# Optimization experiments

Hardware: AMD Instinct MI355X
Metric: run time of the kernel (lower is better)

Reference implementation:

```python
import jax, jax.numpy as jnp
import numpy as np

NUM_HEAD = 16
EMBED_DIM = 1024
HEAD_DIM = EMBED_DIM // NUM_HEAD
QK_DIM = EMBED_DIM  # qk_dim defaults to embed_dim


def setup_inputs() -> dict:
    key = jax.random.key(0)
    k1, k2, k3 = jax.random.split(key, 3)
    x = jax.random.normal(k1, (4, 2048, EMBED_DIM), dtype=jnp.float32)
    # xavier_uniform-like init scale
    lim_qkv = float(np.sqrt(6.0 / (EMBED_DIM + 3 * EMBED_DIM)))
    lim_out = float(np.sqrt(6.0 / (EMBED_DIM + EMBED_DIM)))
    W_QKV = jax.random.uniform(k2, (EMBED_DIM, 3 * EMBED_DIM), jnp.float32, -lim_qkv, lim_qkv)
    W_Out = jax.random.uniform(k3, (EMBED_DIM, EMBED_DIM), jnp.float32, -lim_out, lim_out)
    return {"x": x, "W_QKV": W_QKV, "W_Out": W_Out}


def reference(x, W_QKV, W_Out):
    bsz, slen, _ = x.shape
    # [b,s,3E] -> [b,s,H,hd,3] -> [b,H,s,hd,3]  (interleaved qkv layout, as in torch source)
    qkv = (x @ W_QKV).reshape(bsz, slen, NUM_HEAD, HEAD_DIM, 3).transpose(0, 2, 1, 3, 4)
    q, k, v = qkv[..., 0], qkv[..., 1], qkv[..., 2]
    # NOTE: module scales by sqrt(qk_dim) (full dim), not sqrt(head_dim)
    scores = jnp.einsum("bhqd,bhkd->bhqk", q, k) / np.sqrt(QK_DIM).astype(np.float32)
    attn = jax.nn.softmax(scores, axis=-1)  # dropout p=0.0 -> identity
    out = jnp.einsum("bhqk,bhkd->bhqd", attn, v)  # [b,H,s,hd]
    out = out.transpose(0, 2, 1, 3).reshape(bsz, slen, EMBED_DIM)
    return out @ W_Out
```

## Files before the change

kernel.cpp:

```cpp
#include <hip/hip_runtime.h>
#include <stdint.h>

typedef __bf16 bf16x8 __attribute__((ext_vector_type(8)));
typedef __bf16 bf16x4_t __attribute__((ext_vector_type(4)));
typedef float f32x4 __attribute__((ext_vector_type(4)));
typedef unsigned short u16x8 __attribute__((ext_vector_type(8)));
typedef unsigned short u16x4 __attribute__((ext_vector_type(4)));
typedef short s16x4 __attribute__((ext_vector_type(4)));
typedef unsigned int u32x2 __attribute__((ext_vector_type(2)));

#if __has_builtin(__builtin_amdgcn_mfma_f32_16x16x16bf16_1k)
#define MFMA16X16X16(a, b, c) __builtin_amdgcn_mfma_f32_16x16x16bf16_1k((a), (b), (c), 0, 0, 0)
#elif __has_builtin(__builtin_amdgcn_mfma_f32_16x16x16_bf16)
#define MFMA16X16X16(a, b, c)                                                             \
    __builtin_amdgcn_mfma_f32_16x16x16_bf16(__builtin_bit_cast(bf16x4_t, (a)),            \
                                            __builtin_bit_cast(bf16x4_t, (b)), (c), 0, 0, 0)
#else
static __device__ __forceinline__ f32x4 MFMA16X16X16(s16x4, s16x4, f32x4 c) { return c; }
#endif

#if __has_builtin(__builtin_amdgcn_exp2f)
#define EXP2(x) __builtin_amdgcn_exp2f(x)
#else
#define EXP2(x) exp2f(x)
#endif

__device__ __forceinline__ unsigned short f2bf(float f) {
    unsigned int u = __float_as_uint(f);
    u += 0x7fffu + ((u >> 16) & 1u);
    return (unsigned short)(u >> 16);
}

__device__ __forceinline__ int swz64(int row, int c) {
    return (c & 7) | ((((c >> 3) ^ row) & 7) << 3);
}

__device__ __forceinline__ void glds16(const unsigned short* g, unsigned short* l) {
    __builtin_amdgcn_global_load_lds((const __attribute__((address_space(1))) void*)g,
                                     (__attribute__((address_space(3))) void*)l, 16, 0, 0);
}

__device__ __forceinline__ void transpose_body(const float* __restrict__ in,
                                               unsigned short* __restrict__ out,
                                               unsigned short (*tile)[33],
                                               int K, int N, int permute, int nb, int kb) {
    int tx = threadIdx.x & 31, ty = threadIdx.x >> 5;
    #pragma unroll
    for (int r = ty; r < 32; r += 8)
        tile[r][tx] = f2bf(in[(size_t)(kb + r) * N + nb + tx]);
    __syncthreads();
    #pragma unroll
    for (int r = ty; r < 32; r += 8) {
        int n_orig = nb + r, col = kb + tx;
        int row;
        if (permute) {
            int h = n_orig / 192, rem = n_orig - h * 192;
            int d = rem / 3, cc = rem - 3 * d;
            row = cc * 1024 + h * 64 + d;
        } else {
            row = n_orig;
        }
        out[(size_t)row * K + (col & ~63) + swz64(row, col & 63)] = tile[tx][r];
    }
}

__global__ __launch_bounds__(256) void preprocess_kernel(const float* __restrict__ x,
                                                         const float* __restrict__ wqkv,
                                                         const float* __restrict__ wout,
                                                         unsigned short* __restrict__ xb,
                                                         unsigned short* __restrict__ wqkvt,
                                                         unsigned short* __restrict__ woutt) {
    __shared__ unsigned short tile[32][33];
    int bid = blockIdx.x;
    if (bid < 4096) {
        size_t id = (size_t)bid * 256 + threadIdx.x;
        int row = (int)(id >> 7);
        int cid = (int)(id & 127);
        const float4* src = (const float4*)(x + id * 8);
        float4 a = src[0], b = src[1];
        u16x8 o;
        o[0] = f2bf(a.x); o[1] = f2bf(a.y); o[2] = f2bf(a.z); o[3] = f2bf(a.w);
        o[4] = f2bf(b.x); o[5] = f2bf(b.y); o[6] = f2bf(b.z); o[7] = f2bf(b.w);
        int group = cid >> 3, ch = cid & 7;
        *(u16x8*)(xb + (size_t)row * 1024 + group * 64 + (((ch ^ row) & 7) << 3)) = o;
    } else if (bid < 7168) {
        int idx = bid - 4096;
        transpose_body(wqkv, wqkvt, tile, 1024, 3072, 1, (idx % 96) * 32, (idx / 96) * 32);
    } else {
        int idx = bid - 7168;
        transpose_body(wout, woutt, tile, 1024, 1024, 0, (idx % 32) * 32, (idx / 32) * 32);
    }
}

__device__ __forceinline__ void gemm128_mainloop(const unsigned short* __restrict__ A,
                                                 const unsigned short* __restrict__ Bt,
                                                 f32x4 acc[4][4]) {
    __shared__ unsigned short smem[4 * 128 * 64];
    const int t = threadIdx.x, lane = t & 63, w = t >> 6;
    const int wm = w & 1, wn = w >> 1;
    const int r16 = lane & 15, quad = lane >> 4;
    const size_t mb = (size_t)blockIdx.y * 128, nb = (size_t)blockIdx.x * 128;

    const f32x4 zf = {0.f, 0.f, 0.f, 0.f};
    #pragma unroll
    for (int i = 0; i < 4; i++)
        #pragma unroll
        for (int j = 0; j < 4; j++) acc[i][j] = zf;

    int aoff[2], boff[2];
    #pragma unroll
    for (int kkh = 0; kkh < 2; kkh++) {
        int chunk = ((kkh * 4 + quad) ^ (r16 & 7)) << 3;
        aoff[kkh] = (wm * 64 + r16) * 64 + chunk;
        boff[kkh] = (wn * 64 + r16) * 64 + chunk;
    }

    const unsigned short* ap = A + (mb + w * 32 + (lane >> 3)) * 1024 + (lane & 7) * 8;
    const unsigned short* bp = Bt + (nb + w * 32 + (lane >> 3)) * 1024 + (lane & 7) * 8;
    unsigned short* al = smem + w * 2048;
    unsigned short* bl = smem + 16384 + w * 2048;
    auto stage = [&](int reg) {
        #pragma unroll
        for (int c = 0; c < 4; c++) {
            glds16(ap + c * 8192, al + reg * 8192 + c * 512);
            glds16(bp + c * 8192, bl + reg * 8192 + c * 512);
        }
        ap += 64;
        bp += 64;
    };

    auto body = [&](const unsigned short* as, const unsigned short* bs) {
        #pragma unroll
        for (int kkh = 0; kkh < 2; kkh++) {
            bf16x8 af[4], bfv[4];
            #pragma unroll
            for (int i = 0; i < 4; i++) af[i] = *(const bf16x8*)(as + i * 1024 + aoff[kkh]);
            #pragma unroll
            for (int j = 0; j < 4; j++) bfv[j] = *(const bf16x8*)(bs + j * 1024 + boff[kkh]);
            #pragma unroll
            for (int i = 0; i < 4; i++)
                #pragma unroll
                for (int j = 0; j < 4; j++)
                    acc[i][j] =
                        __builtin_amdgcn_mfma_f32_16x16x32_bf16(af[i], bfv[j], acc[i][j], 0, 0, 0);
        }
    };

    const unsigned short* A0 = smem;
    const unsigned short* A1 = smem + 8192;
    const unsigned short* B0 = smem + 16384;
    const unsigned short* B1 = smem + 24576;

    stage(0);
    #pragma unroll 1
    for (int j = 0; j < 7; j++) {
        __syncthreads();
        stage(1);
        body(A0, B0);
        __syncthreads();
        stage(0);
        body(A1, B1);
    }
    __syncthreads();
    stage(1);
    body(A0, B0);
    __syncthreads();
    body(A1, B1);
}

__global__ __launch_bounds__(256) void gemm_qkv_kernel(const unsigned short* __restrict__ A,
                                                       const unsigned short* __restrict__ Bt,
                                                       unsigned short* __restrict__ Qo,
                                                       unsigned short* __restrict__ Ko,
                                                       unsigned short* __restrict__ Vo) {
    f32x4 acc[4][4];
    gemm128_mainloop(A, Bt, acc);
    const int t = threadIdx.x, lane = t & 63, w = t >> 6;
    const int wm = w & 1, wn = w >> 1;
    const int c16 = lane & 15, quad = lane >> 4;
    const int mb = blockIdx.y * 128, nb = blockIdx.x * 128;
    const int cls = nb >> 10;
    const int hh = ((nb & 1023) >> 6) + wn;
    const float SCALE_Q = 1.4426950408889634f / 32.0f;
    #pragma unroll
    for (int i = 0; i < 4; i++) {
        #pragma unroll
        for (int r = 0; r < 4; r++) {
            int m = mb + wm * 64 + i * 16 + quad * 4 + r;
            int b = m >> 11, s = m & 2047;
            int bh = b * 16 + hh;
            #pragma unroll
            for (int j = 0; j < 4; j++) {
                int d = j * 16 + c16;
                float v = acc[i][j][r];
                if (cls == 0)
                    Qo[((size_t)bh * 2048 + s) * 64 + swz64(s, d)] = f2bf(v * SCALE_Q);
                else if (cls == 1)
                    Ko[((size_t)bh * 2048 + s) * 64 + swz64(s, d)] = f2bf(v);
                else
                    Vo[((size_t)bh * 64 + d) * 2048 + (s & ~63) + swz64(d, s & 63)] = f2bf(v);
            }
        }
    }
}

__global__ __launch_bounds__(256) void gemm_out_kernel(const unsigned short* __restrict__ A,
                                                       const unsigned short* __restrict__ Bt,
                                                       float* __restrict__ C) {
    f32x4 acc[4][4];
    gemm128_mainloop(A, Bt, acc);
    const int t = threadIdx.x, lane = t & 63, w = t >> 6;
    const int wm = w & 1, wn = w >> 1;
    const int c16 = lane & 15, quad = lane >> 4;
    const int mb = blockIdx.y * 128, nb = blockIdx.x * 128;
    #pragma unroll
    for (int i = 0; i < 4; i++)
        #pragma unroll
        for (int j = 0; j < 4; j++)
            #pragma unroll
            for (int r = 0; r < 4; r++) {
                int m = mb + wm * 64 + i * 16 + quad * 4 + r;
                int n = nb + wn * 64 + j * 16 + c16;
                C[(size_t)m * 1024 + n] = acc[i][j][r];
            }
}

__global__ __launch_bounds__(256) void attn_kernel(const unsigned short* __restrict__ Qg,
                                                   const unsigned short* __restrict__ Kg,
                                                   const unsigned short* __restrict__ Vt,
                                                   unsigned short* __restrict__ O) {
    __shared__ unsigned short smem[4 * 64 * 64];
    unsigned short* K0 = smem;
    unsigned short* K1 = smem + 4096;
    unsigned short* V0 = smem + 8192;
    unsigned short* V1 = smem + 12288;
    const int t = threadIdx.x, lane = t & 63, w = t >> 6;
    const int c16 = lane & 15, quad = lane >> 4;
    const int bh = blockIdx.y, q0 = blockIdx.x * 128;

    bf16x8 qf[2][2];
    #pragma unroll
    for (int qt = 0; qt < 2; qt++) {
        int row = q0 + w * 32 + qt * 16 + c16;
        #pragma unroll
        for (int kkh = 0; kkh < 2; kkh++) {
            int c = kkh * 32 + quad * 8;
            qf[qt][kkh] = *(const bf16x8*)(Qg + ((size_t)bh * 2048 + row) * 64 + swz64(row, c));
        }
    }

    int koff[2], voff[4];
    #pragma unroll
    for (int kkh = 0; kkh < 2; kkh++)
        koff[kkh] = c16 * 64 + ((((kkh * 4 + quad) ^ c16) & 7) << 3);
    #pragma unroll
    for (int kt = 0; kt < 4; kt++)
        voff[kt] = c16 * 64 + (quad & 1) * 4 + ((((kt * 2 + (quad >> 1)) ^ c16) & 7) << 3);

    const unsigned short* kgp =
        Kg + ((size_t)bh * 2048 + w * 16 + (lane >> 3)) * 64 + (lane & 7) * 8;
    const unsigned short* vgp =
        Vt + ((size_t)bh * 64 + w * 16 + (lane >> 3)) * 2048 + (lane & 7) * 8;
    unsigned short* kl = smem + (w * 16) * 64;
    auto stage = [&](int reg) {
        #pragma unroll
        for (int c = 0; c < 2; c++) {
            glds16(kgp + c * 512, kl + reg * 4096 + c * 512);
            glds16(vgp + c * 16384, kl + 8192 + reg * 4096 + c * 512);
        }
        kgp += 4096;
        vgp += 64;
    };

    const f32x4 zf = {0.f, 0.f, 0.f, 0.f};
    f32x4 acc_o[2][4];
    float den[2] = {0.f, 0.f};
    #pragma unroll
    for (int qt = 0; qt < 2; qt++)
        #pragma unroll
        for (int dt = 0; dt < 4; dt++) acc_o[qt][dt] = zf;

    auto body = [&](const unsigned short* ks, const unsigned short* vs) {
        f32x4 sacc[4][2];
        {
            bf16x8 kf[4];
            #pragma unroll
            for (int kt = 0; kt < 4; kt++)
                kf[kt] = *(const bf16x8*)(ks + kt * 1024 + koff[0]);
            #pragma unroll
            for (int kt = 0; kt < 4; kt++)
                #pragma unroll
                for (int qt = 0; qt < 2; qt++)
                    sacc[kt][qt] =
                        __builtin_amdgcn_mfma_f32_16x16x32_bf16(kf[kt], qf[qt][0], zf, 0, 0, 0);
        }
        {
            bf16x8 kf[4];
            #pragma unroll
            for (int kt = 0; kt < 4; kt++)
                kf[kt] = *(const bf16x8*)(ks + kt * 1024 + koff[1]);
            #pragma unroll
            for (int kt = 0; kt < 4; kt++)
                #pragma unroll
                for (int qt = 0; qt < 2; qt++)
                    sacc[kt][qt] = __builtin_amdgcn_mfma_f32_16x16x32_bf16(kf[kt], qf[qt][1],
                                                                           sacc[kt][qt], 0, 0, 0);
        }
        #pragma unroll
        for (int kt = 0; kt < 4; kt++) {
            s16x4 vf[4];
            #pragma unroll
            for (int dt = 0; dt < 4; dt++)
                vf[dt] = *(const s16x4*)(vs + dt * 1024 + voff[kt]);
            #pragma unroll
            for (int qt = 0; qt < 2; qt++) {
                float e0 = EXP2(sacc[kt][qt][0]);
                float e1 = EXP2(sacc[kt][qt][1]);
                float e2 = EXP2(sacc[kt][qt][2]);
                float e3 = EXP2(sacc[kt][qt][3]);
                den[qt] += (e0 + e1) + (e2 + e3);
                bf16x4_t pb = {(__bf16)e0, (__bf16)e1, (__bf16)e2, (__bf16)e3};
                s16x4 pk = __builtin_bit_cast(s16x4, pb);
                #pragma unroll
                for (int dt = 0; dt < 4; dt++)
                    acc_o[qt][dt] = MFMA16X16X16(pk, vf[dt], acc_o[qt][dt]);
            }
        }
    };

    stage(0);
    #pragma unroll 1
    for (int it2 = 0; it2 < 15; it2++) {
        __syncthreads();
        stage(1);
        body(K0, V0);
        __syncthreads();
        stage(0);
        body(K1, V1);
    }
    __syncthreads();
    stage(1);
    body(K0, V0);
    __syncthreads();
    body(K1, V1);

    #pragma unroll
    for (int qt = 0; qt < 2; qt++) {
        den[qt] += __shfl_xor(den[qt], 16);
        den[qt] += __shfl_xor(den[qt], 32);
    }

    const int b = bh >> 4, h = bh & 15;
    #pragma unroll
    for (int qt = 0; qt < 2; qt++) {
        #pragma unroll
        for (int r = 0; r < 4; r++) {
            float rd = 1.0f / __shfl(den[qt], quad * 4 + r);
            int srow = q0 + w * 32 + qt * 16 + quad * 4 + r;
            #pragma unroll
            for (int dt = 0; dt < 4; dt++) {
                int col = dt * 16 + c16;
                O[((size_t)b * 2048 + srow) * 1024 + h * 64 + swz64(srow, col)] =
                    f2bf(acc_o[qt][dt][r] * rd);
            }
        }
    }
}

extern "C" void kernel_launch(void* const* d_in, const int* in_sizes, int n_in,
                              void* d_out, int out_size, void* d_ws, size_t ws_size,
                              hipStream_t stream) {
    (void)in_sizes; (void)n_in; (void)out_size; (void)ws_size;
    const float* x = (const float*)d_in[0];
    const float* wqkv = (const float*)d_in[1];
    const float* wout = (const float*)d_in[2];
    float* out = (float*)d_out;

    const size_t SZ_X = 8388608;
    const size_t SZ_WQKV = 3145728;
    const size_t SZ_WOUT = 1048576;

    unsigned short* ws = (unsigned short*)d_ws;
    unsigned short* xb = ws;
    unsigned short* wqkvt = xb + SZ_X;
    unsigned short* woutt = wqkvt + SZ_WQKV;
    unsigned short* Qa = woutt + SZ_WOUT;
    unsigned short* Ka = Qa + SZ_X;
    unsigned short* Va = Ka + SZ_X;
    unsigned short* attn = Va + SZ_X;

    preprocess_kernel<<<8192, 256, 0, stream>>>(x, wqkv, wout, xb, wqkvt, woutt);
    gemm_qkv_kernel<<<dim3(24, 64), 256, 0, stream>>>(xb, wqkvt, Qa, Ka, Va);
    attn_kernel<<<dim3(16, 64), 256, 0, stream>>>(Qa, Ka, Va, attn);
    gemm_out_kernel<<<dim3(8, 64), 256, 0, stream>>>(attn, woutt, out);
}
```

Baseline: 279.6 us.

## Use 16x16x32 MFMA for PV with permuted V layout and raise MFMA priority

Changes how the V projection is stored so each lane's 8 keys line up with the two score tiles. This lets the P·V product use 16x16x32 bf16 MFMA with a single 16-byte LDS read, replacing the 16x16x16 MFMA with 8-byte reads, and halves the number of PV MFMA instructions. It also wraps the MFMA blocks in the GEMM and attention kernels with s_setprio to favour matrix issue across waves. The risk is a mismatch between the new permutation and the fragment layout, plus some extra register pressure from holding 8-wide P fragments.

```diff
diff --git a/kernel.cpp b/kernel.cpp
--- a/kernel.cpp
+++ b/kernel.cpp
@@ -9,22 +9,18 @@
 typedef short s16x4 __attribute__((ext_vector_type(4)));
 typedef unsigned int u32x2 __attribute__((ext_vector_type(2)));
 
-#if __has_builtin(__builtin_amdgcn_mfma_f32_16x16x16bf16_1k)
-#define MFMA16X16X16(a, b, c) __builtin_amdgcn_mfma_f32_16x16x16bf16_1k((a), (b), (c), 0, 0, 0)
-#elif __has_builtin(__builtin_amdgcn_mfma_f32_16x16x16_bf16)
-#define MFMA16X16X16(a, b, c)                                                             \
-    __builtin_amdgcn_mfma_f32_16x16x16_bf16(__builtin_bit_cast(bf16x4_t, (a)),            \
-                                            __builtin_bit_cast(bf16x4_t, (b)), (c), 0, 0, 0)
-#else
-static __device__ __forceinline__ f32x4 MFMA16X16X16(s16x4, s16x4, f32x4 c) { return c; }
-#endif
-
 #if __has_builtin(__builtin_amdgcn_exp2f)
 #define EXP2(x) __builtin_amdgcn_exp2f(x)
 #else
 #define EXP2(x) exp2f(x)
 #endif
 
+#if __has_builtin(__builtin_amdgcn_s_setprio)
+#define SETPRIO(n) __builtin_amdgcn_s_setprio(n)
+#else
+#define SETPRIO(n)
+#endif
+
 __device__ __forceinline__ unsigned short f2bf(float f) {
     unsigned int u = __float_as_uint(f);
     u += 0x7fffu + ((u >> 16) & 1u);
@@ -33,6 +29,11 @@
 
 __device__ __forceinline__ int swz64(int row, int c) {
     return (c & 7) | ((((c >> 3) ^ row) & 7) << 3);
+}
+
+__device__ __forceinline__ int vperm64(int d, int s) {
+    int chunk = ((s >> 5) << 2) + ((s >> 2) & 3);
+    return (((s >> 4) & 1) << 2) + (s & 3) + (((chunk ^ d) & 7) << 3);
 }
 
 __device__ __forceinline__ void glds16(const unsigned short* g, unsigned short* l) {
@@ -137,12 +138,14 @@
             for (int i = 0; i < 4; i++) af[i] = *(const bf16x8*)(as + i * 1024 + aoff[kkh]);
             #pragma unroll
             for (int j = 0; j < 4; j++) bfv[j] = *(const bf16x8*)(bs + j * 1024 + boff[kkh]);
+            SETPRIO(1);
             #pragma unroll
             for (int i = 0; i < 4; i++)
                 #pragma unroll
                 for (int j = 0; j < 4; j++)
                     acc[i][j] =
                         __builtin_amdgcn_mfma_f32_16x16x32_bf16(af[i], bfv[j], acc[i][j], 0, 0, 0);
+            SETPRIO(0);
         }
     };
 
@@ -198,7 +201,7 @@
                 else if (cls == 1)
                     Ko[((size_t)bh * 2048 + s) * 64 + swz64(s, d)] = f2bf(v);
                 else
-                    Vo[((size_t)bh * 64 + d) * 2048 + (s & ~63) + swz64(d, s & 63)] = f2bf(v);
+                    Vo[((size_t)bh * 64 + d) * 2048 + (s & ~63) + vperm64(d, s & 63)] = f2bf(v);
             }
         }
     }
@@ -249,13 +252,10 @@
         }
     }
 
-    int koff[2], voff[4];
-    #pragma unroll
-    for (int kkh = 0; kkh < 2; kkh++)
-        koff[kkh] = c16 * 64 + ((((kkh * 4 + quad) ^ c16) & 7) << 3);
-    #pragma unroll
-    for (int kt = 0; kt < 4; kt++)
-        voff[kt] = c16 * 64 + (quad & 1) * 4 + ((((kt * 2 + (quad >> 1)) ^ c16) & 7) << 3);
+    int coff[2];
+    #pragma unroll
+    for (int h = 0; h < 2; h++)
+        coff[h] = c16 * 64 + ((((h * 4 + quad) ^ c16) & 7) << 3);
 
     const unsigned short* kgp =
         Kg + ((size_t)bh * 2048 + w * 16 + (lane >> 3)) * 64 + (lane & 7) * 8;
@@ -286,44 +286,55 @@
             bf16x8 kf[4];
             #pragma unroll
             for (int kt = 0; kt < 4; kt++)
-                kf[kt] = *(const bf16x8*)(ks + kt * 1024 + koff[0]);
+                kf[kt] = *(const bf16x8*)(ks + kt * 1024 + coff[0]);
+            SETPRIO(1);
             #pragma unroll
             for (int kt = 0; kt < 4; kt++)
                 #pragma unroll
                 for (int qt = 0; qt < 2; qt++)
                     sacc[kt][qt] =
                         __builtin_amdgcn_mfma_f32_16x16x32_bf16(kf[kt], qf[qt][0], zf, 0, 0, 0);
+            SETPRIO(0);
         }
         {
             bf16x8 kf[4];
             #pragma unroll
             for (int kt = 0; kt < 4; kt++)
-                kf[kt] = *(const bf16x8*)(ks + kt * 1024 + koff[1]);
+                kf[kt] = *(const bf16x8*)(ks + kt * 1024 + coff[1]);
+            SETPRIO(1);
             #pragma unroll
             for (int kt = 0; kt < 4; kt++)
                 #pragma unroll
                 for (int qt = 0; qt < 2; qt++)
                     sacc[kt][qt] = __builtin_amdgcn_mfma_f32_16x16x32_bf16(kf[kt], qf[qt][1],
                                                                            sacc[kt][qt], 0, 0, 0);
-        }
-        #pragma unroll
-        for (int kt = 0; kt < 4; kt++) {
-            s16x4 vf[4];
+            SETPRIO(0);
+        }
+        #pragma unroll
+        for (int g = 0; g < 2; g++) {
+            bf16x8 vf[4];
             #pragma unroll
             for (int dt = 0; dt < 4; dt++)
-                vf[dt] = *(const s16x4*)(vs + dt * 1024 + voff[kt]);
+                vf[dt] = *(const bf16x8*)(vs + dt * 1024 + coff[g]);
             #pragma unroll
             for (int qt = 0; qt < 2; qt++) {
-                float e0 = EXP2(sacc[kt][qt][0]);
-                float e1 = EXP2(sacc[kt][qt][1]);
-                float e2 = EXP2(sacc[kt][qt][2]);
-                float e3 = EXP2(sacc[kt][qt][3]);
-                den[qt] += (e0 + e1) + (e2 + e3);
-                bf16x4_t pb = {(__bf16)e0, (__bf16)e1, (__bf16)e2, (__bf16)e3};
-                s16x4 pk = __builtin_bit_cast(s16x4, pb);
+                float e0 = EXP2(sacc[2 * g][qt][0]);
+                float e1 = EXP2(sacc[2 * g][qt][1]);
+                float e2 = EXP2(sacc[2 * g][qt][2]);
+                float e3 = EXP2(sacc[2 * g][qt][3]);
+                float e4 = EXP2(sacc[2 * g + 1][qt][0]);
+                float e5 = EXP2(sacc[2 * g + 1][qt][1]);
+                float e6 = EXP2(sacc[2 * g + 1][qt][2]);
+                float e7 = EXP2(sacc[2 * g + 1][qt][3]);
+                den[qt] += ((e0 + e1) + (e2 + e3)) + ((e4 + e5) + (e6 + e7));
+                bf16x8 pb = {(__bf16)e0, (__bf16)e1, (__bf16)e2, (__bf16)e3,
+                             (__bf16)e4, (__bf16)e5, (__bf16)e6, (__bf16)e7};
+                SETPRIO(1);
                 #pragma unroll
                 for (int dt = 0; dt < 4; dt++)
-                    acc_o[qt][dt] = MFMA16X16X16(pk, vf[dt], acc_o[qt][dt]);
+                    acc_o[qt][dt] =
+                        __builtin_amdgcn_mfma_f32_16x16x32_bf16(pb, vf[dt], acc_o[qt][dt], 0, 0, 0);
+                SETPRIO(0);
             }
         }
     };
```

After: 283.0 us. About the same (+1.2%).
